# Kernel optimization log

Hardware: AMD Instinct MI355X
Metric: run time of the kernel (lower is better)

## Reference

```python
import jax, jax.numpy as jnp
import numpy as np

B, N, F = 2048, 65536, 128
NUM_K = 3
NUM_LABELS = 10
EXPONENT = 2.0


def setup_inputs() -> dict:
    key = jax.random.key(0)
    k1, k2, k3 = jax.random.split(key, 3)
    # positive inputs: tf.pow with a float exponent NaNs on negative bases
    x_input = jax.random.uniform(k1, (B, F), dtype=jnp.float32)
    train_inputs = jax.random.uniform(k2, (N, F), dtype=jnp.float32)
    train_labels = jax.random.randint(k3, (N,), 0, NUM_LABELS, dtype=jnp.int32)
    features = jnp.ones((F,), dtype=jnp.float32)  # abe_features, ones init
    return {
        "x_input": x_input,
        "train_inputs": train_inputs,
        "train_labels": train_labels,
        "features": features,
    }


def reference(x_input, train_inputs, train_labels, features):
    # weighted_inputs = features * train_inputs
    w = features[None, :] * train_inputs  # [N, F]

    # Minkowsky distance (faithful to the TF graph):
    # (sum(x^p) + sum(w^p))^(1/p) - 2 * x @ w^T
    left = jnp.sum(x_input ** EXPONENT, axis=1)[:, None]   # [B, 1]
    right = jnp.sum(w ** EXPONENT, axis=1)[None, :]        # [1, N]
    distance = (left + right) ** (1.0 / EXPONENT) - 2.0 * (x_input @ w.T)  # [B, N]

    # top-k nearest neighbors via top_k of negated distances
    values, indices = jax.lax.top_k(-distance, NUM_K)      # [B, K]

    # gather neighbor labels and average (tf.reduce_mean on int = floor div)
    labels = train_labels[indices]                          # [B, K] int32
    outputs = jnp.sum(labels, axis=1) // NUM_K              # [B] int32
    one_hot = jax.nn.one_hot(outputs, NUM_LABELS, dtype=jnp.float32)  # [B, NUM_LABELS]

    return (one_hot, values, indices, labels)
```

## Files before the change

kernel.cpp:

```cpp
#include <hip/hip_runtime.h>
#include <hip/hip_bf16.h>
#include <cstdint>
#include <cstddef>

typedef short bf16x8 __attribute__((ext_vector_type(8)));
typedef float f32x4 __attribute__((ext_vector_type(4)));

namespace {
constexpr int kB = 2048;
constexpr int kN = 65536;
constexpr int kF = 128;
constexpr int kLabels = 10;
constexpr int kIMax = 0x7fffffff;

constexpr int BM = 128;
constexpr int BN = 256;
constexpr int SLICE = 2048;
constexpr int NTILES = SLICE / BN;
constexpr int NCH = 4;
constexpr int NCHT = NTILES * NCH;
constexpr int NSUB = kN / 32;
constexpr float kMargin = 0.25f;
}

#define TOP3_INSERT(dd, ii, D0, I0, D1, I1, D2, I2)                              \
  do {                                                                           \
    float _d = (dd); int _i = (ii);                                              \
    if (_d < (D0) || (_d == (D0) && _i < (I0))) {                                \
      (D2) = (D1); (I2) = (I1); (D1) = (D0); (I1) = (I0); (D0) = _d; (I0) = _i;  \
    } else if (_d < (D1) || (_d == (D1) && _i < (I1))) {                         \
      (D2) = (D1); (I2) = (I1); (D1) = _d; (I1) = _i;                            \
    } else if (_d < (D2) || (_d == (D2) && _i < (I2))) {                         \
      (D2) = _d; (I2) = _i;                                                      \
    }                                                                            \
  } while (0)

__device__ inline unsigned short f2bf(float a) {
  __hip_bfloat16 h = __float2bfloat16(a);
  return __builtin_bit_cast(unsigned short, h);
}

__device__ inline void gload_lds16(const void* g, void* l) {
  __builtin_amdgcn_global_load_lds(
      (const __attribute__((address_space(1))) void*)g,
      (__attribute__((address_space(3))) void*)l, 16, 0, 0);
}

__global__ __launch_bounds__(256) void pack_sumsq_kernel(
    const float* __restrict__ x, const float* __restrict__ train,
    const float* __restrict__ features, unsigned short* __restrict__ Ap,
    unsigned short* __restrict__ Bp, float* __restrict__ left,
    float* __restrict__ right) {
  const int wid = (int)((blockIdx.x * 256 + threadIdx.x) >> 6);
  const int lane = threadIdx.x & 63;
  if (wid >= kB + kN) return;
  const float2 fv = reinterpret_cast<const float2*>(features)[lane];
  const float* src;
  unsigned short* dst;
  float pm0, pm1, sm0, sm1;
  if (wid < kB) {
    src = x + (size_t)wid * kF;
    dst = Ap + (size_t)wid * 128;
    pm0 = fv.x; pm1 = fv.y;
    sm0 = 1.0f; sm1 = 1.0f;
  } else {
    src = train + (size_t)(wid - kB) * kF;
    dst = Bp + (size_t)(wid - kB) * 128;
    pm0 = 1.0f; pm1 = 1.0f;
    sm0 = fv.x; sm1 = fv.y;
  }
  const float2 v = reinterpret_cast<const float2*>(src)[lane];
  const float pa = v.x * pm0, pb = v.y * pm1;
  const float sa = v.x * sm0, sb = v.y * sm1;
  const unsigned short ha = f2bf(pa), hb = f2bf(pb);
  reinterpret_cast<unsigned int*>(dst)[lane] = (unsigned int)ha | ((unsigned int)hb << 16);
  float s = sa * sa + sb * sb;
  #pragma unroll
  for (int m = 1; m <= 32; m <<= 1) s += __shfl_xor(s, m);
  if (lane == 0) {
    if (wid < kB) left[wid] = s;
    else right[wid - kB] = s;
  }
}

__global__ __launch_bounds__(256, 2) void knn_main_kernel(
    const unsigned short* __restrict__ Ap, const unsigned short* __restrict__ Bp,
    const float* __restrict__ left, const float* __restrict__ right,
    float* __restrict__ minbuf) {
  __shared__ alignas(16) unsigned short lsA[3][BM * 32];
  __shared__ alignas(16) unsigned short lsB[3][BN * 32];
  __shared__ alignas(16) float lsR[SLICE];

  const int slice = blockIdx.x;
  const int mb = blockIdx.y;
  const int row0 = mb * BM;
  const int col0 = slice * SLICE;
  const int t = threadIdx.x;
  const int lane = t & 63;
  const int wm = (t >> 6) >> 1;
  const int wn = (t >> 6) & 1;

  #pragma unroll
  for (int i = 0; i < 2; ++i)
    reinterpret_cast<float4*>(lsR)[t + i * 256] =
        reinterpret_cast<const float4*>(right + col0)[t + i * 256];

  float lrow[4][4];
  #pragma unroll
  for (int mf = 0; mf < 4; ++mf)
    #pragma unroll
    for (int rg = 0; rg < 4; ++rg)
      lrow[mf][rg] = left[row0 + wm * 64 + mf * 16 + (lane >> 4) * 4 + rg];

  const int rr = t >> 2;
  const int p = t & 3;
  size_t gbaseA[2], gbaseB[4];
  int ldsoffA[2], ldsoffB[4];
  #pragma unroll
  for (int i = 0; i < 2; ++i) {
    const int r = i * 64 + rr;
    const int ps = p ^ ((r >> 1) & 3);
    gbaseA[i] = (size_t)(row0 + r) * 256 + (size_t)ps * 16;
    ldsoffA[i] = i * 4096 + t * 16;
  }
  #pragma unroll
  for (int i = 0; i < 4; ++i) {
    const int r = i * 64 + rr;
    const int ps = p ^ ((r >> 1) & 3);
    gbaseB[i] = (size_t)(col0 + r) * 256 + (size_t)ps * 16;
    ldsoffB[i] = i * 4096 + t * 16;
  }

  int offA[4], offB[8];
  #pragma unroll
  for (int mf = 0; mf < 4; ++mf) {
    const int rl = wm * 64 + mf * 16 + (lane & 15);
    offA[mf] = rl * 64 + (((lane >> 4) ^ ((rl >> 1) & 3)) * 16);
  }
  #pragma unroll
  for (int nf = 0; nf < 8; ++nf) {
    const int cl = wn * 128 + nf * 16 + (lane & 15);
    offB[nf] = cl * 64 + (((lane >> 4) ^ ((cl >> 1) & 3)) * 16);
  }

  const char* ApB = (const char*)Ap;
  const char* BpB = (const char*)Bp;

  auto stage = [&](int buf, int c, int nt) {
    char* lA = (char*)&lsA[buf][0];
    char* lB = (char*)&lsB[buf][0];
    #pragma unroll
    for (int i = 0; i < 2; ++i)
      gload_lds16(ApB + gbaseA[i] + (size_t)c * 64, lA + ldsoffA[i]);
    #pragma unroll
    for (int i = 0; i < 4; ++i)
      gload_lds16(BpB + gbaseB[i] + (size_t)nt * 65536 + (size_t)c * 64, lB + ldsoffB[i]);
  };

  asm volatile("s_waitcnt vmcnt(0) lgkmcnt(0)" ::: "memory");
  __syncthreads();

  stage(0, 0, 0);
  stage(1, 1, 0);

  const bool bwriter = (lane & 3) == 0;

  int g = 0;
  for (int nt = 0; nt < NTILES; ++nt) {
    f32x4 acc[4][8];
    #pragma unroll
    for (int mf = 0; mf < 4; ++mf)
      #pragma unroll
      for (int nf = 0; nf < 8; ++nf)
        acc[mf][nf] = (f32x4){0.f, 0.f, 0.f, 0.f};

    for (int c = 0; c < NCH; ++c, ++g) {
      if (g + 2 < NCHT)
        stage((g + 2) % 3, (g + 2) & 3, (g + 2) >> 2);
      if (g <= NCHT - 3)       asm volatile("s_waitcnt vmcnt(12)" ::: "memory");
      else if (g == NCHT - 2)  asm volatile("s_waitcnt vmcnt(6)" ::: "memory");
      else                     asm volatile("s_waitcnt vmcnt(0)" ::: "memory");
      __builtin_amdgcn_s_barrier();
      asm volatile("" ::: "memory");

      const char* lA = (const char*)&lsA[g % 3][0];
      const char* lB = (const char*)&lsB[g % 3][0];
      bf16x8 a[4], b[8];
      #pragma unroll
      for (int mf = 0; mf < 4; ++mf)
        a[mf] = *reinterpret_cast<const bf16x8*>(lA + offA[mf]);
      #pragma unroll
      for (int nf = 0; nf < 8; ++nf)
        b[nf] = *reinterpret_cast<const bf16x8*>(lB + offB[nf]);
      __builtin_amdgcn_s_setprio(1);
      #pragma unroll
      for (int mf = 0; mf < 4; ++mf)
        #pragma unroll
        for (int nf = 0; nf < 8; ++nf)
          acc[mf][nf] = __builtin_amdgcn_mfma_f32_16x16x32_bf16(
              a[mf], b[nf], acc[mf][nf], 0, 0, 0);
      __builtin_amdgcn_s_setprio(0);
      asm volatile("" ::: "memory");
      __builtin_amdgcn_s_barrier();
      asm volatile("" ::: "memory");
    }

    float rj[8];
    #pragma unroll
    for (int nf = 0; nf < 8; ++nf)
      rj[nf] = lsR[nt * 256 + wn * 128 + nf * 16 + (lane & 15)];
    const int binbase = slice * 64 + nt * 8 + wn * 4 + ((lane >> 2) & 3);
    #pragma unroll
    for (int mf = 0; mf < 4; ++mf) {
      #pragma unroll
      for (int rg = 0; rg < 4; ++rg) {
        const float l = lrow[mf][rg];
        float d[8];
        #pragma unroll
        for (int nf = 0; nf < 8; ++nf)
          d[nf] = sqrtf(l + rj[nf]) - 2.0f * acc[mf][nf][rg];
        d[0] = fminf(d[0], d[4]); d[1] = fminf(d[1], d[5]);
        d[2] = fminf(d[2], d[6]); d[3] = fminf(d[3], d[7]);
        d[0] = fminf(d[0], d[2]); d[1] = fminf(d[1], d[3]);
        float v = fminf(d[0], d[1]);
        v = fminf(v, __shfl_xor(v, 1));
        v = fminf(v, __shfl_xor(v, 2));
        if (bwriter) {
          const int row = row0 + wm * 64 + mf * 16 + (lane >> 4) * 4 + rg;
          minbuf[(size_t)row * NSUB + binbase] = v;
        }
      }
    }
  }
}

__global__ __launch_bounds__(256) void select_rescore_kernel(
    const float* __restrict__ x, const float* __restrict__ train,
    const float* __restrict__ features, const float* __restrict__ left,
    const float* __restrict__ right, const int* __restrict__ labels,
    const float* __restrict__ minbuf, float* __restrict__ out) {
  __shared__ float Xs[4][kF];
  const int t = threadIdx.x;
  if (t < 128) {
    const int rr = t >> 5, q = t & 31;
    float4 xv = reinterpret_cast<const float4*>(
        x + (size_t)(blockIdx.x * 4 + rr) * kF)[q];
    const float4 f = reinterpret_cast<const float4*>(features)[q];
    xv.x *= f.x; xv.y *= f.y; xv.z *= f.z; xv.w *= f.w;
    reinterpret_cast<float4*>(&Xs[rr][0])[q] = xv;
  }
  __syncthreads();
  const int wave = t >> 6, lane = t & 63;
  const int row = blockIdx.x * 4 + wave;
  const float lr = left[row];
  const float* mrow = minbuf + (size_t)row * NSUB;

  float v0 = __builtin_inff(), v1 = v0, v2 = v0;
  #pragma unroll 4
  for (int i = 0; i < NSUB / 64; ++i) {
    const float m = mrow[i * 64 + lane];
    if (m < v0) { v2 = v1; v1 = v0; v0 = m; }
    else if (m < v1) { v2 = v1; v1 = m; }
    else if (m < v2) { v2 = m; }
  }
  #pragma unroll
  for (int msk = 1; msk <= 32; msk <<= 1) {
    const float e0 = __shfl_xor(v0, msk), e1 = __shfl_xor(v1, msk), e2 = __shfl_xor(v2, msk);
    if (e0 < v0) { v2 = v1; v1 = v0; v0 = e0; } else if (e0 < v1) { v2 = v1; v1 = e0; } else if (e0 < v2) v2 = e0;
    if (e1 < v0) { v2 = v1; v1 = v0; v0 = e1; } else if (e1 < v1) { v2 = v1; v1 = e1; } else if (e1 < v2) v2 = e1;
    if (e2 < v0) { v2 = v1; v1 = v0; v0 = e2; } else if (e2 < v1) { v2 = v1; v1 = e2; } else if (e2 < v2) v2 = e2;
  }
  const float tau = v2 + kMargin;

  float d0 = __builtin_inff(), d1 = d0, d2 = d0;
  int i0 = kIMax, i1 = kIMax, i2 = kIMax;
  for (int base = 0; base < NSUB; base += 64) {
    const float m = mrow[base + lane];
    unsigned long long msk = __ballot(m <= tau);
    while (msk) {
      const int bpos = __builtin_ctzll(msk);
      msk &= msk - 1;
      const int sub = base + bpos;
      if (lane < 32) {
        const int j = (sub >> 2) * 128 + (lane >> 2) * 16 + (sub & 3) * 4 + (lane & 3);
        const float4* wp = reinterpret_cast<const float4*>(train + (size_t)j * kF);
        float acc = 0.f;
        #pragma unroll 8
        for (int kq = 0; kq < 32; ++kq) {
          const float4 w4 = wp[kq];
          const float4 x4 = reinterpret_cast<const float4*>(&Xs[wave][0])[kq];
          acc = fmaf(x4.w, w4.w, fmaf(x4.z, w4.z, fmaf(x4.y, w4.y, fmaf(x4.x, w4.x, acc))));
        }
        const float d = sqrtf(lr + right[j]) - 2.0f * acc;
        TOP3_INSERT(d, j, d0, i0, d1, i1, d2, i2);
      }
    }
  }
  #pragma unroll
  for (int msk = 1; msk <= 32; msk <<= 1) {
    const float e0 = __shfl_xor(d0, msk), e1 = __shfl_xor(d1, msk), e2 = __shfl_xor(d2, msk);
    const int f0 = __shfl_xor(i0, msk), f1 = __shfl_xor(i1, msk), f2 = __shfl_xor(i2, msk);
    TOP3_INSERT(e0, f0, d0, i0, d1, i1, d2, i2);
    TOP3_INSERT(e1, f1, d0, i0, d1, i1, d2, i2);
    TOP3_INSERT(e2, f2, d0, i0, d1, i1, d2, i2);
  }
  if (lane == 0) {
    const int l0 = labels[i0], l1 = labels[i1], l2 = labels[i2];
    const int o = (l0 + l1 + l2) / 3;
    float* one_hot = out;
    float* values = out + (size_t)kB * kLabels;
    float* indices = values + (size_t)kB * 3;
    float* labs = indices + (size_t)kB * 3;
    #pragma unroll
    for (int c = 0; c < kLabels; ++c)
      one_hot[(size_t)row * kLabels + c] = (c == o) ? 1.0f : 0.0f;
    values[row * 3 + 0] = -d0; values[row * 3 + 1] = -d1; values[row * 3 + 2] = -d2;
    indices[row * 3 + 0] = (float)i0; indices[row * 3 + 1] = (float)i1; indices[row * 3 + 2] = (float)i2;
    labs[row * 3 + 0] = (float)l0; labs[row * 3 + 1] = (float)l1; labs[row * 3 + 2] = (float)l2;
  }
}

extern "C" void kernel_launch(void* const* d_in, const int* in_sizes, int n_in,
                              void* d_out, int out_size, void* d_ws, size_t ws_size,
                              hipStream_t stream) {
  const float* x = (const float*)d_in[0];
  const float* train = (const float*)d_in[1];
  const int* labels = (const int*)d_in[2];
  const float* features = (const float*)d_in[3];
  float* out = (float*)d_out;

  char* ws = (char*)d_ws;
  unsigned short* Bp = (unsigned short*)ws;
  unsigned short* Ap = (unsigned short*)(ws + 16777216);
  float* left = (float*)(ws + 17301504);
  float* right = (float*)(ws + 17309696);
  float* minbuf = (float*)(ws + 17571840);

  pack_sumsq_kernel<<<((kB + kN) * 64 + 255) / 256, 256, 0, stream>>>(
      x, train, features, Ap, Bp, left, right);
  knn_main_kernel<<<dim3(32, 16), 256, 0, stream>>>(Ap, Bp, left, right, minbuf);
  select_rescore_kernel<<<kB / 4, 256, 0, stream>>>(
      x, train, features, left, right, labels, minbuf, out);
}
```

Before: 306.5 us.

## Make B column panel stationary in LDS and stream all query rows

Each block now keeps a 128-column training panel resident in LDS, together with all left norms, and loops over all 2048 query rows in 128-row panels, streaming only A through a triple buffer. The grid becomes 512 one-dimensional blocks instead of 32x16, and each wave's tile shrinks from 64x128 to 64x64. The min-buffer granularity is refined to 16-column sub-bins, which doubles minbuf size but makes rescoring candidates tighter (16 per bin instead of 32). The trade is less MFMA work per LDS load, more minbuf writes, and different occupancy from the larger LDS footprint.

```diff
diff --git a/kernel.cpp b/kernel.cpp
--- a/kernel.cpp
+++ b/kernel.cpp
@@ -13,13 +13,12 @@
 constexpr int kLabels = 10;
 constexpr int kIMax = 0x7fffffff;
 
-constexpr int BM = 128;
-constexpr int BN = 256;
-constexpr int SLICE = 2048;
-constexpr int NTILES = SLICE / BN;
+constexpr int BCOLS = 128;
+constexpr int PROWS = 128;
+constexpr int NPANEL = kB / PROWS;
 constexpr int NCH = 4;
-constexpr int NCHT = NTILES * NCH;
-constexpr int NSUB = kN / 32;
+constexpr int NG = NPANEL * NCH;
+constexpr int NSUB = kN / 16;
 constexpr float kMargin = 0.25f;
 }
 
@@ -87,14 +86,13 @@
     const unsigned short* __restrict__ Ap, const unsigned short* __restrict__ Bp,
     const float* __restrict__ left, const float* __restrict__ right,
     float* __restrict__ minbuf) {
-  __shared__ alignas(16) unsigned short lsA[3][BM * 32];
-  __shared__ alignas(16) unsigned short lsB[3][BN * 32];
-  __shared__ alignas(16) float lsR[SLICE];
+  __shared__ alignas(16) unsigned short lsB[NCH * BCOLS * 32];
+  __shared__ alignas(16) unsigned short lsA[3][PROWS * 32];
+  __shared__ float lsL[kB];
+  __shared__ float lsR[BCOLS];
 
   const int slice = blockIdx.x;
-  const int mb = blockIdx.y;
-  const int row0 = mb * BM;
-  const int col0 = slice * SLICE;
+  const int col0 = slice * BCOLS;
   const int t = threadIdx.x;
   const int lane = t & 63;
   const int wm = (t >> 6) >> 1;
@@ -102,101 +100,106 @@
 
   #pragma unroll
   for (int i = 0; i < 2; ++i)
-    reinterpret_cast<float4*>(lsR)[t + i * 256] =
-        reinterpret_cast<const float4*>(right + col0)[t + i * 256];
-
-  float lrow[4][4];
-  #pragma unroll
-  for (int mf = 0; mf < 4; ++mf)
-    #pragma unroll
-    for (int rg = 0; rg < 4; ++rg)
-      lrow[mf][rg] = left[row0 + wm * 64 + mf * 16 + (lane >> 4) * 4 + rg];
+    reinterpret_cast<float4*>(lsL)[t + i * 256] =
+        reinterpret_cast<const float4*>(left)[t + i * 256];
+  if (t < BCOLS / 4)
+    reinterpret_cast<float4*>(lsR)[t] =
+        reinterpret_cast<const float4*>(right + col0)[t];
 
   const int rr = t >> 2;
   const int p = t & 3;
-  size_t gbaseA[2], gbaseB[4];
-  int ldsoffA[2], ldsoffB[4];
+  size_t aoff[2], boff[2];
+  int ldsoff[2];
   #pragma unroll
   for (int i = 0; i < 2; ++i) {
     const int r = i * 64 + rr;
     const int ps = p ^ ((r >> 1) & 3);
-    gbaseA[i] = (size_t)(row0 + r) * 256 + (size_t)ps * 16;
-    ldsoffA[i] = i * 4096 + t * 16;
-  }
-  #pragma unroll
-  for (int i = 0; i < 4; ++i) {
-    const int r = i * 64 + rr;
-    const int ps = p ^ ((r >> 1) & 3);
-    gbaseB[i] = (size_t)(col0 + r) * 256 + (size_t)ps * 16;
-    ldsoffB[i] = i * 4096 + t * 16;
-  }
-
-  int offA[4], offB[8];
+    aoff[i] = (size_t)r * 256 + (size_t)ps * 16;
+    boff[i] = (size_t)(col0 + r) * 256 + (size_t)ps * 16;
+    ldsoff[i] = i * 4096 + t * 16;
+  }
+
+  int offA[2], offB[4];
+  #pragma unroll
+  for (int mf = 0; mf < 4; ++mf) {
+    if (mf < 2) {}
+  }
+  int offAf[4], offBf[4];
   #pragma unroll
   for (int mf = 0; mf < 4; ++mf) {
     const int rl = wm * 64 + mf * 16 + (lane & 15);
-    offA[mf] = rl * 64 + (((lane >> 4) ^ ((rl >> 1) & 3)) * 16);
-  }
-  #pragma unroll
-  for (int nf = 0; nf < 8; ++nf) {
-    const int cl = wn * 128 + nf * 16 + (lane & 15);
-    offB[nf] = cl * 64 + (((lane >> 4) ^ ((cl >> 1) & 3)) * 16);
+    offAf[mf] = rl * 64 + (((lane >> 4) ^ ((rl >> 1) & 3)) * 16);
+  }
+  #pragma unroll
+  for (int nf = 0; nf < 4; ++nf) {
+    const int cl = wn * 64 + nf * 16 + (lane & 15);
+    offBf[nf] = cl * 64 + (((lane >> 4) ^ ((cl >> 1) & 3)) * 16);
   }
 
   const char* ApB = (const char*)Ap;
   const char* BpB = (const char*)Bp;
 
-  auto stage = [&](int buf, int c, int nt) {
+  auto stageA = [&](int buf, int g) {
+    const int mp = g >> 2, c = g & 3;
     char* lA = (char*)&lsA[buf][0];
-    char* lB = (char*)&lsB[buf][0];
     #pragma unroll
     for (int i = 0; i < 2; ++i)
-      gload_lds16(ApB + gbaseA[i] + (size_t)c * 64, lA + ldsoffA[i]);
-    #pragma unroll
-    for (int i = 0; i < 4; ++i)
-      gload_lds16(BpB + gbaseB[i] + (size_t)nt * 65536 + (size_t)c * 64, lB + ldsoffB[i]);
+      gload_lds16(ApB + aoff[i] + (size_t)mp * 32768 + (size_t)c * 64,
+                  lA + ldsoff[i]);
   };
 
-  asm volatile("s_waitcnt vmcnt(0) lgkmcnt(0)" ::: "memory");
+  {
+    char* lB = (char*)&lsB[0];
+    #pragma unroll
+    for (int c = 0; c < NCH; ++c)
+      #pragma unroll
+      for (int i = 0; i < 2; ++i)
+        gload_lds16(BpB + boff[i] + (size_t)c * 64, lB + c * 8192 + ldsoff[i]);
+  }
+  stageA(0, 0);
+  stageA(1, 1);
   __syncthreads();
 
-  stage(0, 0, 0);
-  stage(1, 1, 0);
+  float rj[4];
+  #pragma unroll
+  for (int nf = 0; nf < 4; ++nf)
+    rj[nf] = lsR[wn * 64 + nf * 16 + (lane & 15)];
 
   const bool bwriter = (lane & 3) == 0;
-
-  int g = 0;
-  for (int nt = 0; nt < NTILES; ++nt) {
-    f32x4 acc[4][8];
+  const int subbase = slice * 8 + wn * 4 + ((lane >> 2) & 3);
+
+  for (int mp = 0; mp < NPANEL; ++mp) {
+    f32x4 acc[4][4];
     #pragma unroll
     for (int mf = 0; mf < 4; ++mf)
       #pragma unroll
-      for (int nf = 0; nf < 8; ++nf)
+      for (int nf = 0; nf < 4; ++nf)
         acc[mf][nf] = (f32x4){0.f, 0.f, 0.f, 0.f};
 
-    for (int c = 0; c < NCH; ++c, ++g) {
-      if (g + 2 < NCHT)
-        stage((g + 2) % 3, (g + 2) & 3, (g + 2) >> 2);
-      if (g <= NCHT - 3)       asm volatile("s_waitcnt vmcnt(12)" ::: "memory");
-      else if (g == NCHT - 2)  asm volatile("s_waitcnt vmcnt(6)" ::: "memory");
-      else                     asm volatile("s_waitcnt vmcnt(0)" ::: "memory");
+    for (int c = 0; c < NCH; ++c) {
+      const int g = mp * 4 + c;
+      if (g < NG - 2) stageA((g + 2) % 3, g + 2);
+      if (g < NG - 2)       asm volatile("s_waitcnt vmcnt(4)" ::: "memory");
+      else if (g == NG - 2) asm volatile("s_waitcnt vmcnt(2)" ::: "memory");
+      else                  asm volatile("s_waitcnt vmcnt(0)" ::: "memory");
       __builtin_amdgcn_s_barrier();
       asm volatile("" ::: "memory");
 
       const char* lA = (const char*)&lsA[g % 3][0];
-      const char* lB = (const char*)&lsB[g % 3][0];
-      bf16x8 a[4], b[8];
+      const char* lB = (const char*)&lsB[c * 4096 * 2 / 2];
+      lB = (const char*)&lsB[0] + c * 8192;
+      bf16x8 a[4], b[4];
       #pragma unroll
       for (int mf = 0; mf < 4; ++mf)
-        a[mf] = *reinterpret_cast<const bf16x8*>(lA + offA[mf]);
-      #pragma unroll
-      for (int nf = 0; nf < 8; ++nf)
-        b[nf] = *reinterpret_cast<const bf16x8*>(lB + offB[nf]);
+        a[mf] = *reinterpret_cast<const bf16x8*>(lA + offAf[mf]);
+      #pragma unroll
+      for (int nf = 0; nf < 4; ++nf)
+        b[nf] = *reinterpret_cast<const bf16x8*>(lB + offBf[nf]);
       __builtin_amdgcn_s_setprio(1);
       #pragma unroll
       for (int mf = 0; mf < 4; ++mf)
         #pragma unroll
-        for (int nf = 0; nf < 8; ++nf)
+        for (int nf = 0; nf < 4; ++nf)
           acc[mf][nf] = __builtin_amdgcn_mfma_f32_16x16x32_bf16(
               a[mf], b[nf], acc[mf][nf], 0, 0, 0);
       __builtin_amdgcn_s_setprio(0);
@@ -205,30 +208,22 @@
       asm volatile("" ::: "memory");
     }
 
-    float rj[8];
-    #pragma unroll
-    for (int nf = 0; nf < 8; ++nf)
-      rj[nf] = lsR[nt * 256 + wn * 128 + nf * 16 + (lane & 15)];
-    const int binbase = slice * 64 + nt * 8 + wn * 4 + ((lane >> 2) & 3);
+    const int prow0 = mp * PROWS + wm * 64;
     #pragma unroll
     for (int mf = 0; mf < 4; ++mf) {
       #pragma unroll
       for (int rg = 0; rg < 4; ++rg) {
-        const float l = lrow[mf][rg];
-        float d[8];
-        #pragma unroll
-        for (int nf = 0; nf < 8; ++nf)
-          d[nf] = sqrtf(l + rj[nf]) - 2.0f * acc[mf][nf][rg];
-        d[0] = fminf(d[0], d[4]); d[1] = fminf(d[1], d[5]);
-        d[2] = fminf(d[2], d[6]); d[3] = fminf(d[3], d[7]);
-        d[0] = fminf(d[0], d[2]); d[1] = fminf(d[1], d[3]);
-        float v = fminf(d[0], d[1]);
+        const int row = prow0 + mf * 16 + (lane >> 4) * 4 + rg;
+        const float l = lsL[row];
+        float d0 = sqrtf(l + rj[0]) - 2.0f * acc[mf][0][rg];
+        float d1 = sqrtf(l + rj[1]) - 2.0f * acc[mf][1][rg];
+        float d2 = sqrtf(l + rj[2]) - 2.0f * acc[mf][2][rg];
+        float d3 = sqrtf(l + rj[3]) - 2.0f * acc[mf][3][rg];
+        float v = fminf(fminf(d0, d1), fminf(d2, d3));
         v = fminf(v, __shfl_xor(v, 1));
         v = fminf(v, __shfl_xor(v, 2));
-        if (bwriter) {
-          const int row = row0 + wm * 64 + mf * 16 + (lane >> 4) * 4 + rg;
-          minbuf[(size_t)row * NSUB + binbase] = v;
-        }
+        if (bwriter)
+          minbuf[(size_t)row * NSUB + subbase] = v;
       }
     }
   }
@@ -281,8 +276,9 @@
       const int bpos = __builtin_ctzll(msk);
       msk &= msk - 1;
       const int sub = base + bpos;
-      if (lane < 32) {
-        const int j = (sub >> 2) * 128 + (lane >> 2) * 16 + (sub & 3) * 4 + (lane & 3);
+      if (lane < 16) {
+        const int j = (sub >> 3) * 128 + ((sub >> 2) & 1) * 64 +
+                      (lane >> 2) * 16 + (sub & 3) * 4 + (lane & 3);
         const float4* wp = reinterpret_cast<const float4*>(train + (size_t)j * kF);
         float acc = 0.f;
         #pragma unroll 8
@@ -338,7 +334,7 @@
 
   pack_sumsq_kernel<<<((kB + kN) * 64 + 255) / 256, 256, 0, stream>>>(
       x, train, features, Ap, Bp, left, right);
-  knn_main_kernel<<<dim3(32, 16), 256, 0, stream>>>(Ap, Bp, left, right, minbuf);
+  knn_main_kernel<<<kN / BCOLS, 256, 0, stream>>>(Ap, Bp, left, right, minbuf);
   select_rescore_kernel<<<kB / 4, 256, 0, stream>>>(
       x, train, features, left, right, labels, minbuf, out);
 }
```

New measurement: 284.5 us. 7.2% less time.
